# Kernel optimization log

Hardware: AMD Instinct MI355X
Metric: run time of the kernel (lower is better)

## Reference

```python
import jax, jax.numpy as jnp
import numpy as np

V, E, H, Z = 32000, 512, 1024, 256
B, S, T = 64, 256, 64
BOS_ID, EOS_ID = 1, 2


def gru_cell(x_gates, h, W_hh, b_hh):
    # torch GRU gate order: r, z, n. x_gates: (B,3H) precomputed W_ih@x+b_ih.
    hg = h @ W_hh.T + b_hh
    xr, xz, xn = jnp.split(x_gates, 3, axis=-1)
    hr, hz, hn = jnp.split(hg, 3, axis=-1)
    r = jax.nn.sigmoid(xr + hr)
    z = jax.nn.sigmoid(xz + hz)
    n = jnp.tanh(xn + r * hn)
    return (1.0 - z) * n + z * h


def setup_inputs() -> dict:
    key = jax.random.key(0)
    ks = jax.random.split(key, 24)
    u = lambda k, sh: jax.random.uniform(k, sh, jnp.float32, -0.1, 0.1)
    n = lambda k, sh: jax.random.normal(k, sh, jnp.float32) * 0.05
    inp = {
        'input': jax.random.randint(ks[0], (S, B), 0, V),
        'eps': jax.random.normal(ks[1], (B, Z), jnp.float32),
        'emb_enc': u(ks[2], (V, E)).at[0].set(0.0),  # padding_idx=0
        'Wih_e': n(ks[3], (3 * H, E)), 'Whh_e': n(ks[4], (3 * H, H)),
        'bih_e': n(ks[5], (3 * H,)), 'bhh_e': n(ks[6], (3 * H,)),
        'W_enc': n(ks[7], (Z, H)), 'b_enc': n(ks[8], (Z,)),
        'W_loc': n(ks[9], (Z, Z)), 'b_loc': n(ks[10], (Z,)),
        'W_scale': n(ks[11], (Z, Z)), 'b_scale': n(ks[12], (Z,)),
        'emb_dec': u(ks[13], (V, E)).at[0].set(0.0),
        'W_dec': n(ks[14], (H, Z)), 'b_dec': n(ks[15], (H,)),
        'Wih_d': n(ks[16], (3 * H, E)), 'Whh_d': n(ks[17], (3 * H, H)),
        'bih_d': n(ks[18], (3 * H,)), 'bhh_d': n(ks[19], (3 * H,)),
        'W_voc': n(ks[20], (V, H)), 'b_voc': n(ks[21], (V,)),
    }
    return inp


def reference(input, eps, emb_enc, Wih_e, Whh_e, bih_e, bhh_e,
              W_enc, b_enc, W_loc, b_loc, W_scale, b_scale,
              emb_dec, W_dec, b_dec, Wih_d, Whh_d, bih_d, bhh_d,
              W_voc, b_voc):
    # ---- encode ----
    x = emb_enc[input]                                   # (S,B,E)
    gx = jnp.einsum('sbe,ge->sbg', x, Wih_e) + bih_e     # (S,B,3H)
    h0 = jnp.zeros((B, H), x.dtype)
    h_last, _ = jax.lax.scan(lambda h, g: (gru_cell(g, h, Whh_e, bhh_e), None), h0, gx)
    henc = h_last @ W_enc.T + b_enc                      # (B,Z)
    loc = henc @ W_loc.T + b_loc
    scale = jax.nn.softplus(henc @ W_scale.T + b_scale)
    # ---- reparametrize ----
    z = loc + eps * jnp.exp(0.5 * scale)
    # ---- decode (fixed T steps; original loop is data-dependent on EOS) ----
    hidden = z @ W_dec.T + b_dec                         # (B,H)
    xd = jnp.broadcast_to(emb_dec[EOS_ID], (B, E))       # constant EOS input each step
    gxd = xd @ Wih_d.T + bih_d                           # (B,3H), hoisted out of loop

    def step(h, _):
        h2 = gru_cell(gxd, h, Whh_d, bhh_d)
        log_p = jax.nn.log_softmax(h2 @ W_voc.T + b_voc, axis=-1)  # (B,V)
        tok = jnp.argmax(log_p)  # global flat argmax, as torch.argmax(...).item()
        return h2, (log_p, tok)

    _, (log_p, toks) = jax.lax.scan(step, hidden, None, length=T)
    seq = jnp.concatenate([jnp.array([BOS_ID], toks.dtype), toks])
    return log_p, seq, loc, scale
```

## Files before the change

kernel.cpp:

```cpp
#include <hip/hip_runtime.h>
#include <math.h>
#include <stdint.h>
#include <stddef.h>

typedef unsigned short u16;
typedef unsigned int   u32;
typedef __attribute__((ext_vector_type(8))) short short8;
typedef __attribute__((ext_vector_type(4))) float f32x4;

#define DI __device__ __forceinline__

static constexpr int Vv = 32000, Ee = 512, Hh = 1024, Zz = 256;
static constexpr int Bb = 64, Ss = 256, Tt = 64;
static constexpr int G3 = 3 * Hh;

static constexpr size_t OFF_WHHE  = 0;
static constexpr size_t SZ_WHH    = (size_t)G3 * Hh * 2;
static constexpr size_t OFF_WHHD  = OFF_WHHE + SZ_WHH;
static constexpr size_t OFF_WIHE3 = OFF_WHHD + SZ_WHH;
static constexpr size_t SZ_WIHE3  = (size_t)G3 * (3 * Ee) * 2;
static constexpr size_t OFF_WVOC  = OFF_WIHE3 + SZ_WIHE3;
static constexpr size_t SZ_WVOC   = (size_t)Vv * Hh * 2;
static constexpr size_t OFF_XS    = OFF_WVOC + SZ_WVOC;
static constexpr size_t SZ_XS     = (size_t)Ss * Bb * (3 * Ee) * 2;
static constexpr size_t OFF_GX    = OFF_XS + SZ_XS;
static constexpr size_t SZ_GX     = (size_t)Ss * Bb * G3 * 4;
static constexpr size_t OFF_H2B   = OFF_GX;
static constexpr size_t OFF_H2F   = OFF_GX + SZ_GX;
static constexpr size_t SZ_H2F    = (size_t)Tt * Bb * Hh * 4;
static constexpr size_t OFF_H     = OFF_H2F + SZ_H2F;
static constexpr size_t OFF_GXD   = OFF_H + (size_t)Bb * Hh * 4;
static constexpr size_t OFF_HENC  = OFF_GXD + 12288;
static constexpr size_t OFF_ZB    = OFF_HENC + (size_t)Bb * Zz * 4;
static constexpr size_t OFF_RM    = OFF_ZB + (size_t)Bb * Zz * 4;
static constexpr size_t OFF_SE    = OFF_RM + 16384;
static constexpr size_t OFF_LSE   = OFF_SE + 16384;
static constexpr size_t OFF_BV    = OFF_LSE + 16384;
static constexpr size_t OFF_BI    = OFF_BV + 16384;
static constexpr size_t OFF_CC    = OFF_BI + 16384;
static constexpr size_t OFF_CAND  = OFF_CC + 16384;
static constexpr size_t OFF_BAR   = OFF_CAND + (size_t)4096 * 32 * 4;

static constexpr size_t SZ_HAB    = (size_t)Bb * 2 * Hh * 2;

DI u16 f2bf(float f) {
  u32 u = __float_as_uint(f);
  u32 r = (u + 0x7FFFu + ((u >> 16) & 1u)) >> 16;
  return (u16)r;
}
DI float bf2f(u16 h) { return __uint_as_float(((u32)h) << 16); }

DI f32x4 mfma16(short8 a, short8 b, f32x4 c) {
  return __builtin_amdgcn_mfma_f32_16x16x32_bf16(a, b, c, 0, 0, 0);
}
DI void llds16(const u16* g, u16* l) {
  __builtin_amdgcn_global_load_lds(
      (const __attribute__((address_space(1))) u32*)g,
      (__attribute__((address_space(3))) u32*)l, 16, 0, 0);
}

DI void ag_store_u32(u32* p, u32 v) {
  __hip_atomic_store(p, v, __ATOMIC_RELAXED, __HIP_MEMORY_SCOPE_AGENT);
}

DI u16* hbuf_dev(char* rA, char* rB, char* rC, int i) {
  if (i < 192) return (u16*)(rA + (size_t)i * SZ_HAB);
  if (i < 228) return (u16*)(rB + (size_t)(i - 192) * SZ_HAB);
  return (u16*)(rC + (size_t)(i - 228) * SZ_HAB);
}

__global__ void k_zero(u32* p, int n) {
  for (int i = blockIdx.x * 256 + threadIdx.x; i < n; i += gridDim.x * 256) p[i] = 0;
}

__global__ void k_trip(const float* __restrict__ W, u16* __restrict__ W3, int rows, int kin) {
  int n = rows * kin;
  for (int i = blockIdx.x * 256 + threadIdx.x; i < n; i += gridDim.x * 256) {
    int rr = i / kin, k = i - rr * kin;
    float v = W[i];
    u16 hi = f2bf(v);
    u16 lo = f2bf(v - bf2f(hi));
    u16* o = W3 + (size_t)rr * (3 * kin);
    o[k] = hi; o[kin + k] = hi; o[2 * kin + k] = lo;
  }
}

__global__ void k_tobf(const float* __restrict__ W, u16* __restrict__ Wb, int n) {
  for (int i = blockIdx.x * 256 + threadIdx.x; i < n; i += gridDim.x * 256) Wb[i] = f2bf(W[i]);
}

__global__ void k_xsplit(const int* __restrict__ inp, const float* __restrict__ emb,
                         u16* __restrict__ xs) {
  int n = Ss * Bb * Ee;
  for (int i = blockIdx.x * 256 + threadIdx.x; i < n; i += gridDim.x * 256) {
    int m = i >> 9, k = i & (Ee - 1);
    int tok = inp[m];
    float v = emb[(size_t)tok * Ee + k];
    u16 hi = f2bf(v);
    u16 lo = f2bf(v - bf2f(hi));
    u16* o = xs + (size_t)m * (3 * Ee);
    o[k] = hi; o[Ee + k] = lo; o[2 * Ee + k] = hi;
  }
}

__global__ void k_gxd(const float* __restrict__ emb_dec, const float* __restrict__ Wih_d,
                      const float* __restrict__ bih_d, float* __restrict__ gxd) {
  int g = blockIdx.x * 256 + threadIdx.x;
  if (g >= G3) return;
  const float* er = emb_dec + 2 * Ee;
  const float* wr = Wih_d + (size_t)g * Ee;
  float s = 0.f;
  for (int e = 0; e < Ee; e++) s += er[e] * wr[e];
  gxd[g] = s + bih_d[g];
}

__global__ __launch_bounds__(256, 2) void gemm_bt(
    const u16* __restrict__ A, const u16* __restrict__ Bw, const float* __restrict__ bias,
    float* __restrict__ C, int M, int N, int K) {
  __shared__ __align__(16) u16 As[128 * 32];
  __shared__ __align__(16) u16 Bs[128 * 32];
  int tid = threadIdx.x;
  int wave = tid >> 6, lane = tid & 63;
  int wr = wave >> 1, wc = wave & 1;
  int m0 = blockIdx.y * 128, n0 = blockIdx.x * 128;
  f32x4 acc[4][4];
#pragma unroll
  for (int i = 0; i < 4; i++)
#pragma unroll
    for (int j = 0; j < 4; j++) acc[i][j] = (f32x4){0.f, 0.f, 0.f, 0.f};

  int lrow = lane >> 2, lcol = (lane & 3) * 8;
  int r15 = lane & 15, kk = (lane >> 4) * 8;

  for (int k0 = 0; k0 < K; k0 += 32) {
    __syncthreads();
#pragma unroll
    for (int rch = 0; rch < 2; rch++) {
      int c = rch * 4 + wave;
      int row = c * 16 + lrow;
      llds16(A  + (size_t)(m0 + row) * K + k0 + lcol, &As[c * 512]);
      llds16(Bw + (size_t)(n0 + row) * K + k0 + lcol, &Bs[c * 512]);
    }
    __syncthreads();
    short8 af[4], bfv[4];
#pragma unroll
    for (int mi = 0; mi < 4; mi++)
      af[mi] = *(const short8*)&As[(wr * 64 + mi * 16 + r15) * 32 + kk];
#pragma unroll
    for (int ni = 0; ni < 4; ni++)
      bfv[ni] = *(const short8*)&Bs[(wc * 64 + ni * 16 + r15) * 32 + kk];
#pragma unroll
    for (int mi = 0; mi < 4; mi++)
#pragma unroll
      for (int ni = 0; ni < 4; ni++) acc[mi][ni] = mfma16(af[mi], bfv[ni], acc[mi][ni]);
  }
#pragma unroll
  for (int mi = 0; mi < 4; mi++)
#pragma unroll
    for (int ni = 0; ni < 4; ni++) {
      int col = n0 + wc * 64 + ni * 16 + r15;
      float bs = bias[col];
#pragma unroll
      for (int i = 0; i < 4; i++) {
        int row = m0 + wr * 64 + mi * 16 + (lane >> 4) * 4 + i;
        C[(size_t)row * N + col] = acc[mi][ni][i] + bs;
      }
    }
}

template <int DEC>
__global__ __launch_bounds__(512, 1) void k_pers(
    const u16* __restrict__ W, const float* __restrict__ bhh, const float* __restrict__ gx0,
    char* rA, char* rB, char* rC, float* Hst, float* h2f0, u16* h2b0, int* bar) {
  int tid = threadIdx.x, wave = tid >> 6, lane = tid & 63;
  int r15 = lane & 15, kk = (lane >> 4) * 8;
  int bq = blockIdx.x & 3, jt = blockIdx.x >> 2;
  int b0 = bq * 16, j0 = jt * 16;
  int kbase = wave * 128;
  const int NSTEP = DEC ? Tt : Ss;

  __shared__ float sC[8][64][13];
  __shared__ float hT[256];
  __shared__ __align__(8) u16 stg[2][16][16];

  int bl = tid >> 4, jc = tid & 15;
  float br = 0.f, bz = 0.f, bn = 0.f;
  float xr = 0.f, xz = 0.f, xn = 0.f;
  if (tid < 256) {
    hT[tid] = DEC ? Hst[(size_t)(b0 + bl) * Hh + j0 + jc] : 0.f;
    int j = j0 + jc;
    br = bhh[j]; bz = bhh[Hh + j]; bn = bhh[2 * Hh + j];
    if (DEC) { xr = gx0[j]; xz = gx0[Hh + j]; xn = gx0[2 * Hh + j]; }
    else {
      const float* gr = gx0 + (size_t)(b0 + bl) * G3;
      xr = gr[j]; xz = gr[Hh + j]; xn = gr[2 * Hh + j];
    }
  }
  __syncthreads();

  const u16* Wrow = W + (size_t)(j0 + r15) * Hh + kbase + kk;
  int lsrc = (bl >> 2) * 16 + jc;
  int isrc = bl & 3;

  for (int st = 0; st < NSTEP; st++) {
    const u16* hin = hbuf_dev(rA, rB, rC, st);

    f32x4 acc[3];
#pragma unroll
    for (int g = 0; g < 3; g++) acc[g] = (f32x4){0.f, 0.f, 0.f, 0.f};
    const u16* Ab = hin + (size_t)(b0 + r15) * 2048 + kbase + kk;
#pragma unroll
    for (int ks = 0; ks < 4; ks++) {
      int ko = ks * 32;
      short8 ah = *(const short8*)(Ab + ko);
      short8 al = *(const short8*)(Ab + 1024 + ko);
      short8 w0 = *(const short8*)(Wrow + ko);
      short8 w1 = *(const short8*)(Wrow + (size_t)Hh * Hh + ko);
      short8 w2 = *(const short8*)(Wrow + (size_t)2 * Hh * Hh + ko);
      acc[0] = mfma16(ah, w0, acc[0]);
      acc[1] = mfma16(ah, w1, acc[1]);
      acc[2] = mfma16(ah, w2, acc[2]);
      acc[0] = mfma16(al, w0, acc[0]);
      acc[1] = mfma16(al, w1, acc[1]);
      acc[2] = mfma16(al, w2, acc[2]);
    }
#pragma unroll
    for (int g = 0; g < 3; g++)
#pragma unroll
      for (int i = 0; i < 4; i++) sC[wave][lane][g * 4 + i] = acc[g][i];
    __syncthreads();

    if (tid < 256) {
      float hgr = br, hgz = bz, hgn = bn;
#pragma unroll
      for (int w = 0; w < 8; w++) {
        hgr += sC[w][lsrc][isrc];
        hgz += sC[w][lsrc][4 + isrc];
        hgn += sC[w][lsrc][8 + isrc];
      }
      float rg = 1.0f / (1.0f + expf(-(xr + hgr)));
      float zg = 1.0f / (1.0f + expf(-(xz + hgz)));
      float ng = tanhf(xn + rg * hgn);
      float hn = (1.0f - zg) * ng + zg * hT[tid];
      hT[tid] = hn;
      u16 hi = f2bf(hn), lo = f2bf(hn - bf2f(hi));
      stg[0][bl][jc] = hi;
      stg[1][bl][jc] = lo;
      if (DEC) h2f0[((size_t)st * Bb + b0 + bl) * Hh + j0 + jc] = hn;
    }
    __syncthreads();

    if (tid < 256) {
      int part = tid >> 7, idx = tid & 127, row = idx >> 3, dw = idx & 7;
      if (st + 1 < NSTEP) {
        u16* hout = hbuf_dev(rA, rB, rC, st + 1);
        u32 val = ((const u32*)&stg[part][row][0])[dw];
        ag_store_u32((u32*)(hout + (size_t)(b0 + row) * 2048 + part * 1024 + j0) + dw, val);
      }
      if (DEC && tid < 128) {
        u16* h2b = h2b0 + (size_t)st * Bb * Hh;
        ((u32*)(h2b + (size_t)(b0 + row) * Hh + j0))[dw] = ((const u32*)&stg[0][row][0])[dw];
      }
    }

    if (st + 1 < NSTEP) {
      asm volatile("s_waitcnt vmcnt(0)" ::: "memory");
      __syncthreads();
      if (!DEC && tid < 256) {
        const float* gr = gx0 + ((size_t)(st + 1) * Bb + b0 + bl) * G3;
        int j = j0 + jc;
        xr = gr[j]; xz = gr[Hh + j]; xn = gr[2 * Hh + j];
      }
      if (tid == 0) {
        int g = blockIdx.x & 7;
        int old = __hip_atomic_fetch_add(&bar[g * 16], 1,
                                         __ATOMIC_RELAXED, __HIP_MEMORY_SCOPE_AGENT);
        if (old == 32 * (st + 1) - 1)
          __hip_atomic_fetch_add(&bar[128 + bq * 16], 1,
                                 __ATOMIC_RELAXED, __HIP_MEMORY_SCOPE_AGENT);
        while (__hip_atomic_load(&bar[128 + bq * 16],
                                 __ATOMIC_RELAXED, __HIP_MEMORY_SCOPE_AGENT) < 2 * (st + 1))
          __builtin_amdgcn_s_sleep(1);
      }
      __syncthreads();
    }
  }

  if (!DEC && tid < 256)
    Hst[(size_t)(b0 + bl) * Hh + j0 + jc] = hT[tid];
}

template <int DEC>
__global__ __launch_bounds__(512, 1) void k_step3(
    const u16* __restrict__ W, const float* __restrict__ bhh, const float* __restrict__ gxp,
    const u16* __restrict__ hAin, u16* __restrict__ hAout, float* __restrict__ h,
    float* __restrict__ h2f, u16* __restrict__ h2b) {
  __shared__ float sC[4][64][13];
  int tid = threadIdx.x, wave = tid >> 6, lane = tid & 63;
  int mw = wave & 3, khalf = wave >> 2;
  int m0 = mw * 16;
  int r15 = lane & 15, kk = (lane >> 4) * 8;
  int j0 = blockIdx.x * 16;
  int kbase = khalf * 512;

  f32x4 acc[3];
#pragma unroll
  for (int g = 0; g < 3; g++) acc[g] = (f32x4){0.f, 0.f, 0.f, 0.f};

  const u16* Ah = hAin + (size_t)(m0 + r15) * 2048 + kbase + kk;
  const u16* Wr = W + (size_t)(j0 + r15) * Hh + kbase + kk;
#pragma unroll 4
  for (int ks = 0; ks < 16; ks++) {
    int ko = ks * 32;
    short8 ah = *(const short8*)(Ah + ko);
    short8 al = *(const short8*)(Ah + 1024 + ko);
    short8 b0 = *(const short8*)(Wr + ko);
    short8 b1 = *(const short8*)(Wr + (size_t)Hh * Hh + ko);
    short8 b2 = *(const short8*)(Wr + (size_t)2 * Hh * Hh + ko);
    acc[0] = mfma16(ah, b0, acc[0]);
    acc[1] = mfma16(ah, b1, acc[1]);
    acc[2] = mfma16(ah, b2, acc[2]);
    acc[0] = mfma16(al, b0, acc[0]);
    acc[1] = mfma16(al, b1, acc[1]);
    acc[2] = mfma16(al, b2, acc[2]);
  }

  if (khalf == 1) {
#pragma unroll
    for (int g = 0; g < 3; g++)
#pragma unroll
      for (int i = 0; i < 4; i++) sC[mw][lane][g * 4 + i] = acc[g][i];
  }
  __syncthreads();
  if (khalf == 1) return;

  int j = j0 + r15;
  float br = bhh[j], bz = bhh[Hh + j], bn = bhh[2 * Hh + j];
  float xrD = 0.f, xzD = 0.f, xnD = 0.f;
  if (DEC) { xrD = gxp[j]; xzD = gxp[Hh + j]; xnD = gxp[2 * Hh + j]; }
#pragma unroll
  for (int i = 0; i < 4; i++) {
    int b = m0 + (lane >> 4) * 4 + i;
    float hgr = acc[0][i] + sC[mw][lane][i]     + br;
    float hgz = acc[1][i] + sC[mw][lane][4 + i] + bz;
    float hgn = acc[2][i] + sC[mw][lane][8 + i] + bn;
    float xr, xz, xn;
    if (DEC) { xr = xrD; xz = xzD; xn = xnD; }
    else {
      const float* gr = gxp + (size_t)b * G3;
      xr = gr[j]; xz = gr[Hh + j]; xn = gr[2 * Hh + j];
    }
    float rg = 1.0f / (1.0f + expf(-(xr + hgr)));
    float zg = 1.0f / (1.0f + expf(-(xz + hgz)));
    float ng = tanhf(xn + rg * hgn);
    float hold = h[(size_t)b * Hh + j];
    float hn = (1.0f - zg) * ng + zg * hold;
    h[(size_t)b * Hh + j] = hn;
    u16 hi = f2bf(hn);
    u16 lo = f2bf(hn - bf2f(hi));
    hAout[(size_t)b * 2048 + j] = hi;
    hAout[(size_t)b * 2048 + 1024 + j] = lo;
    if (DEC) {
      h2f[(size_t)b * Hh + j] = hn;
      h2b[(size_t)b * Hh + j] = hi;
    }
  }
}

__global__ __launch_bounds__(256, 2) void k_head1(const float* __restrict__ h,
    const float* __restrict__ Wenc, const float* __restrict__ benc, float* __restrict__ henc) {
  int b = blockIdx.x;
  __shared__ float hs[Hh];
  for (int k = threadIdx.x; k < Hh; k += 256) hs[k] = h[(size_t)b * Hh + k];
  __syncthreads();
  int q = threadIdx.x;
  const float* wrw = Wenc + (size_t)q * Hh;
  float s = 0.f;
  for (int k = 0; k < Hh; k++) s += hs[k] * wrw[k];
  henc[b * Zz + q] = s + benc[q];
}

__global__ __launch_bounds__(256, 2) void k_head2(const float* __restrict__ henc,
    const float* __restrict__ Wloc, const float* __restrict__ bloc,
    const float* __restrict__ Wsc, const float* __restrict__ bsc,
    const float* __restrict__ eps, float* __restrict__ outLoc, float* __restrict__ outSc,
    float* __restrict__ zb) {
  int b = blockIdx.x;
  __shared__ float hs[Zz];
  if (threadIdx.x < Zz) hs[threadIdx.x] = henc[b * Zz + threadIdx.x];
  __syncthreads();
  int q = threadIdx.x;
  const float* wl = Wloc + (size_t)q * Zz;
  const float* wsp = Wsc + (size_t)q * Zz;
  float sl = 0.f, ssum = 0.f;
  for (int k = 0; k < Zz; k++) { sl += hs[k] * wl[k]; ssum += hs[k] * wsp[k]; }
  sl += bloc[q]; ssum += bsc[q];
  float sp = fmaxf(ssum, 0.f) + log1pf(expf(-fabsf(ssum)));
  float zv = sl + eps[b * Zz + q] * expf(0.5f * sp);
  outLoc[b * Zz + q] = sl;
  outSc[b * Zz + q] = sp;
  zb[b * Zz + q] = zv;
}

__global__ __launch_bounds__(256, 2) void k_head3(const float* __restrict__ zb,
    const float* __restrict__ Wdec, const float* __restrict__ bdec,
    float* __restrict__ h, u16* __restrict__ hA0) {
  int b = blockIdx.x;
  __shared__ float zs[Zz];
  if (threadIdx.x < Zz) zs[threadIdx.x] = zb[b * Zz + threadIdx.x];
  __syncthreads();
  for (int j = threadIdx.x; j < Hh; j += 256) {
    const float* wrw = Wdec + (size_t)j * Zz;
    float s = 0.f;
    for (int k = 0; k < Zz; k++) s += zs[k] * wrw[k];
    s += bdec[j];
    h[(size_t)b * Hh + j] = s;
    u16 hi = f2bf(s);
    u16 lo = f2bf(s - bf2f(hi));
    hA0[(size_t)b * 2048 + j] = hi;
    hA0[(size_t)b * 2048 + 1024 + j] = lo;
  }
}

__global__ __launch_bounds__(256, 2) void k_rowred(const float* __restrict__ logits,
    float* __restrict__ rowmax, float* __restrict__ sumexp, int* __restrict__ ccnt,
    int* __restrict__ cand) {
  int r = blockIdx.x;
  const float* row = logits + (size_t)r * Vv;
  __shared__ float red[4];
  __shared__ float srm;
  __shared__ int lcnt;
  __shared__ int lcand[32];
  int tid = threadIdx.x, wave = tid >> 6, lane = tid & 63;
  if (tid == 0) lcnt = 0;
  float m = -3.0e38f;
  for (int c = tid * 4; c < Vv; c += 1024) {
    f32x4 v = *(const f32x4*)(row + c);
    m = fmaxf(fmaxf(fmaxf(m, v.x), v.y), fmaxf(v.z, v.w));
  }
  for (int o = 32; o; o >>= 1) m = fmaxf(m, __shfl_xor(m, o));
  if (lane == 0) red[wave] = m;
  __syncthreads();
  if (tid == 0) srm = fmaxf(fmaxf(red[0], red[1]), fmaxf(red[2], red[3]));
  __syncthreads();
  float rm = srm;
  float s = 0.f;
  for (int c = tid * 4; c < Vv; c += 1024) {
    f32x4 v = *(const f32x4*)(row + c);
    s += expf(v.x - rm) + expf(v.y - rm) + expf(v.z - rm) + expf(v.w - rm);
    if (v.x >= rm - 0.0625f) { int sl = atomicAdd(&lcnt, 1); if (sl < 32) lcand[sl] = c; }
    if (v.y >= rm - 0.0625f) { int sl = atomicAdd(&lcnt, 1); if (sl < 32) lcand[sl] = c + 1; }
    if (v.z >= rm - 0.0625f) { int sl = atomicAdd(&lcnt, 1); if (sl < 32) lcand[sl] = c + 2; }
    if (v.w >= rm - 0.0625f) { int sl = atomicAdd(&lcnt, 1); if (sl < 32) lcand[sl] = c + 3; }
  }
  for (int o = 32; o; o >>= 1) s += __shfl_xor(s, o);
  if (lane == 0) red[wave] = s;
  __syncthreads();
  if (tid == 0) {
    float st = red[0] + red[1] + red[2] + red[3];
    int cc = lcnt < 32 ? lcnt : 32;
    for (int i = 0; i < cc; i++)
      for (int k2 = i + 1; k2 < cc; k2++)
        if (lcand[k2] < lcand[i]) { int t = lcand[i]; lcand[i] = lcand[k2]; lcand[k2] = t; }
    rowmax[r] = rm; sumexp[r] = st; ccnt[r] = cc;
    for (int i = 0; i < cc; i++) cand[r * 32 + i] = lcand[i];
  }
}

__global__ __launch_bounds__(256, 1) void k_refine(const float* __restrict__ logits,
    const float* __restrict__ h2f, const float* __restrict__ Wvoc, const float* __restrict__ bvoc,
    const float* __restrict__ rowmax, const float* __restrict__ sumexp,
    const int* __restrict__ ccnt, const int* __restrict__ cand,
    float* __restrict__ lsec, float* __restrict__ bestv, int* __restrict__ besti) {
  int r = blockIdx.x;
  __shared__ float hrow[Hh];
  __shared__ float lex[32];
  __shared__ float del[32];
  int tid = threadIdx.x, wave = tid >> 6, lane = tid & 63;
  for (int k = tid; k < Hh; k += 256) hrow[k] = h2f[(size_t)r * Hh + k];
  int cnt = ccnt[r];
  float rm = rowmax[r];
  __syncthreads();
  for (int ci = wave; ci < cnt; ci += 4) {
    int v = cand[r * 32 + ci];
    const float* wrw = Wvoc + (size_t)v * Hh;
    float s = 0.f;
    for (int k = lane; k < Hh; k += 64) s += hrow[k] * wrw[k];
    for (int o = 32; o; o >>= 1) s += __shfl_xor(s, o);
    if (lane == 0) {
      float le = s + bvoc[v];
      lex[ci] = le;
      float la = logits[(size_t)r * Vv + v];
      del[ci] = expf(le - rm) - expf(la - rm);
    }
  }
  __syncthreads();
  if (tid == 0) {
    float se = sumexp[r];
    for (int i = 0; i < cnt; i++) se += del[i];
    float lse = rm + logf(se);
    lsec[r] = lse;
    float bv = -3.0e38f; int bvi = 0;
    for (int i = 0; i < cnt; i++)
      if (lex[i] > bv) { bv = lex[i]; bvi = cand[r * 32 + i]; }
    bestv[r] = bv - lse;
    besti[r] = (r & 63) * Vv + bvi;
  }
}

__global__ void k_argmax(const float* __restrict__ bestv, const int* __restrict__ besti,
                         float* __restrict__ outseq) {
  int tid = threadIdx.x;
  if (tid == 0) outseq[0] = 1.0f;
  for (int t = 0; t < Tt; t++) {
    float v = bestv[t * 64 + tid];
    int ii = besti[t * 64 + tid];
    for (int o = 1; o < 64; o <<= 1) {
      float ov = __shfl_xor(v, o);
      int oi = __shfl_xor(ii, o);
      if (ov > v || (ov == v && oi < ii)) { v = ov; ii = oi; }
    }
    if (tid == 0) outseq[1 + t] = (float)ii;
  }
}

__global__ __launch_bounds__(256, 2) void k_logp(float* __restrict__ logits,
                                                 const float* __restrict__ lsec) {
  size_t total = (size_t)Tt * Bb * Vv / 4;
  for (size_t p = (size_t)blockIdx.x * 256 + threadIdx.x; p < total;
       p += (size_t)gridDim.x * 256) {
    int r = (int)(p / (Vv / 4));
    f32x4 v = *(f32x4*)(logits + p * 4);
    float l = lsec[r];
    v.x -= l; v.y -= l; v.z -= l; v.w -= l;
    *(f32x4*)(logits + p * 4) = v;
  }
}

extern "C" void kernel_launch(void* const* d_in, const int* in_sizes, int n_in,
                              void* d_out, int out_size, void* d_ws, size_t ws_size,
                              hipStream_t stream) {
  (void)in_sizes; (void)n_in; (void)out_size; (void)ws_size;
  const int*   inp     = (const int*)d_in[0];
  const float* eps     = (const float*)d_in[1];
  const float* emb_enc = (const float*)d_in[2];
  const float* Wih_e   = (const float*)d_in[3];
  const float* Whh_e   = (const float*)d_in[4];
  const float* bih_e   = (const float*)d_in[5];
  const float* bhh_e   = (const float*)d_in[6];
  const float* W_enc   = (const float*)d_in[7];
  const float* b_enc   = (const float*)d_in[8];
  const float* W_loc   = (const float*)d_in[9];
  const float* b_loc   = (const float*)d_in[10];
  const float* W_sc    = (const float*)d_in[11];
  const float* b_sc    = (const float*)d_in[12];
  const float* emb_dec = (const float*)d_in[13];
  const float* W_dec   = (const float*)d_in[14];
  const float* b_dec   = (const float*)d_in[15];
  const float* Wih_d   = (const float*)d_in[16];
  const float* Whh_d   = (const float*)d_in[17];
  const float* bih_d   = (const float*)d_in[18];
  const float* bhh_d   = (const float*)d_in[19];
  const float* W_voc   = (const float*)d_in[20];
  const float* b_voc   = (const float*)d_in[21];

  char* ws = (char*)d_ws;
  u16*   WHHE  = (u16*)(ws + OFF_WHHE);
  u16*   WHHD  = (u16*)(ws + OFF_WHHD);
  u16*   WIHE3 = (u16*)(ws + OFF_WIHE3);
  u16*   WVOC  = (u16*)(ws + OFF_WVOC);
  u16*   XS    = (u16*)(ws + OFF_XS);
  float* GX    = (float*)(ws + OFF_GX);
  float* Hst   = (float*)(ws + OFF_H);
  float* H2F   = (float*)(ws + OFF_H2F);
  u16*   H2B   = (u16*)(ws + OFF_H2B);
  float* GXD   = (float*)(ws + OFF_GXD);
  float* HENC  = (float*)(ws + OFF_HENC);
  float* ZB    = (float*)(ws + OFF_ZB);
  float* RM    = (float*)(ws + OFF_RM);
  float* SE    = (float*)(ws + OFF_SE);
  float* LSE   = (float*)(ws + OFF_LSE);
  float* BV    = (float*)(ws + OFF_BV);
  int*   BI    = (int*)(ws + OFF_BI);
  int*   CC    = (int*)(ws + OFF_CC);
  int*   CAND  = (int*)(ws + OFF_CAND);
  int*   BAR   = (int*)(ws + OFF_BAR);

  char* rA = ws + OFF_XS;
  char* rB = ws + OFF_WIHE3;
  char* rC = ws + OFF_H2F;
  auto hbuf = [&](int i) -> u16* {
    if (i < 192) return (u16*)(rA + (size_t)i * SZ_HAB);
    if (i < 228) return (u16*)(rB + (size_t)(i - 192) * SZ_HAB);
    return (u16*)(rC + (size_t)(i - 228) * SZ_HAB);
  };

  float* out     = (float*)d_out;
  float* logits  = out;
  float* outseq  = out + (size_t)Tt * Bb * Vv;
  float* outloc  = outseq + (Tt + 1);
  float* outsc   = outloc + Bb * Zz;

  k_tobf<<<1024, 256, 0, stream>>>(Whh_e, WHHE, G3 * Hh);
  k_tobf<<<1024, 256, 0, stream>>>(Whh_d, WHHD, G3 * Hh);
  k_trip<<<512, 256, 0, stream>>>(Wih_e, WIHE3, G3, Ee);
  k_tobf<<<2048, 256, 0, stream>>>(W_voc, WVOC, Vv * Hh);
  k_xsplit<<<2048, 256, 0, stream>>>(inp, emb_enc, XS);

  {
    dim3 g(G3 / 128, (Ss * Bb) / 128);
    gemm_bt<<<g, 256, 0, stream>>>(XS, WIHE3, bih_e, GX, Ss * Bb, G3, 3 * Ee);
  }
  k_gxd<<<12, 256, 0, stream>>>(emb_dec, Wih_d, bih_d, GXD);
  k_zero<<<64, 256, 0, stream>>>((u32*)hbuf(0), (int)(SZ_HAB / 4));
  k_zero<<<1, 256, 0, stream>>>((u32*)BAR, 256);

  hipError_t ce;
  {
    const u16* a0 = WHHE; const float* a1 = bhh_e; const float* a2 = GX;
    char* a3 = rA; char* a4 = rB; char* a5 = rC; float* a6 = Hst;
    float* a7 = nullptr; u16* a8 = nullptr; int* a9 = BAR;
    void* args[] = {&a0,&a1,&a2,&a3,&a4,&a5,&a6,&a7,&a8,&a9};
    ce = hipLaunchCooperativeKernel(reinterpret_cast<void*>(&k_pers<0>),
                                    dim3(256), dim3(512), args, 0, stream);
  }
  if (ce != hipSuccess) {
    for (int s = 0; s < Ss; s++)
      k_step3<0><<<64, 512, 0, stream>>>(WHHE, bhh_e, GX + (size_t)s * Bb * G3,
                                         hbuf(s), hbuf(s + 1), Hst, nullptr, nullptr);
  }

  k_head1<<<64, 256, 0, stream>>>(Hst, W_enc, b_enc, HENC);
  k_head2<<<64, 256, 0, stream>>>(HENC, W_loc, b_loc, W_sc, b_sc, eps, outloc, outsc, ZB);
  k_head3<<<64, 256, 0, stream>>>(ZB, W_dec, b_dec, Hst, hbuf(0));
  k_zero<<<1, 256, 0, stream>>>((u32*)BAR, 256);

  {
    const u16* a0 = WHHD; const float* a1 = bhh_d; const float* a2 = GXD;
    char* a3 = rA; char* a4 = rB; char* a5 = rC; float* a6 = Hst;
    float* a7 = H2F; u16* a8 = H2B; int* a9 = BAR;
    void* args[] = {&a0,&a1,&a2,&a3,&a4,&a5,&a6,&a7,&a8,&a9};
    hipError_t cd = hipLaunchCooperativeKernel(reinterpret_cast<void*>(&k_pers<1>),
                                               dim3(256), dim3(512), args, 0, stream);
    if (cd != hipSuccess) {
      for (int t = 0; t < Tt; t++)
        k_step3<1><<<64, 512, 0, stream>>>(WHHD, bhh_d, GXD, hbuf(t), hbuf(t + 1), Hst,
                                           H2F + (size_t)t * Bb * Hh,
                                           H2B + (size_t)t * Bb * Hh);
    }
  }

  {
    dim3 g(Vv / 128, (Tt * Bb) / 128);
    gemm_bt<<<g, 256, 0, stream>>>(H2B, WVOC, b_voc, logits, Tt * Bb, Vv, Hh);
  }

  k_rowred<<<Tt * Bb, 256, 0, stream>>>(logits, RM, SE, CC, CAND);
  k_refine<<<Tt * Bb, 256, 0, stream>>>(logits, H2F, W_voc, b_voc, RM, SE, CC, CAND, LSE, BV, BI);
  k_argmax<<<1, 64, 0, stream>>>(BV, BI, outseq);
  k_logp<<<2048, 256, 0, stream>>>(logits, LSE);
}
```

Baseline: 2.879 ms.

## Replace atomic-counter grid barrier with per-block flags and per-quarter gather

The persistent GRU kernel's inter-block barrier changes from two-level fetch_add counters to per-block step flags. Block jt==0 of each batch quarter has one wave poll all 64 peer flags and then publish a release flag, which the other blocks of that quarter spin on. The aim is to cut atomic read-modify-write contention and serialization on each of the 256 or 64 recurrent steps. Stores of h2f/h2b become agent-scope atomic stores, and the barrier buffer grows to 4224 words, which must fit inside the reserved workspace region.

```diff
diff --git a/kernel.cpp b/kernel.cpp
--- a/kernel.cpp
+++ b/kernel.cpp
@@ -62,6 +62,12 @@
 DI void ag_store_u32(u32* p, u32 v) {
   __hip_atomic_store(p, v, __ATOMIC_RELAXED, __HIP_MEMORY_SCOPE_AGENT);
 }
+DI u32 ag_load_u32(const u32* p) {
+  return __hip_atomic_load((u32*)p, __ATOMIC_RELAXED, __HIP_MEMORY_SCOPE_AGENT);
+}
+DI void ag_store_f32(float* p, float v) {
+  __hip_atomic_store(p, v, __ATOMIC_RELAXED, __HIP_MEMORY_SCOPE_AGENT);
+}
 
 DI u16* hbuf_dev(char* rA, char* rB, char* rC, int i) {
   if (i < 192) return (u16*)(rA + (size_t)i * SZ_HAB);
@@ -171,7 +177,7 @@
 template <int DEC>
 __global__ __launch_bounds__(512, 1) void k_pers(
     const u16* __restrict__ W, const float* __restrict__ bhh, const float* __restrict__ gx0,
-    char* rA, char* rB, char* rC, float* Hst, float* h2f0, u16* h2b0, int* bar) {
+    char* rA, char* rB, char* rC, float* Hst, float* h2f0, u16* h2b0, u32* bar) {
   int tid = threadIdx.x, wave = tid >> 6, lane = tid & 63;
   int r15 = lane & 15, kk = (lane >> 4) * 8;
   int bq = blockIdx.x & 3, jt = blockIdx.x >> 2;
@@ -201,6 +207,7 @@
   const u16* Wrow = W + (size_t)(j0 + r15) * Hh + kbase + kk;
   int lsrc = (bl >> 2) * 16 + jc;
   int isrc = bl & 3;
+  int flgidx = (lane * 4 + bq) * 16;
 
   for (int st = 0; st < NSTEP; st++) {
     const u16* hin = hbuf_dev(rA, rB, rC, st);
@@ -246,7 +253,7 @@
       u16 hi = f2bf(hn), lo = f2bf(hn - bf2f(hi));
       stg[0][bl][jc] = hi;
       stg[1][bl][jc] = lo;
-      if (DEC) h2f0[((size_t)st * Bb + b0 + bl) * Hh + j0 + jc] = hn;
+      if (DEC) ag_store_f32(&h2f0[((size_t)st * Bb + b0 + bl) * Hh + j0 + jc], hn);
     }
     __syncthreads();
 
@@ -259,27 +266,32 @@
       }
       if (DEC && tid < 128) {
         u16* h2b = h2b0 + (size_t)st * Bb * Hh;
-        ((u32*)(h2b + (size_t)(b0 + row) * Hh + j0))[dw] = ((const u32*)&stg[0][row][0])[dw];
+        ag_store_u32((u32*)(h2b + (size_t)(b0 + row) * Hh + j0) + dw,
+                     ((const u32*)&stg[0][row][0])[dw]);
       }
     }
 
     if (st + 1 < NSTEP) {
       asm volatile("s_waitcnt vmcnt(0)" ::: "memory");
       __syncthreads();
+      if (tid == 0)
+        ag_store_u32(&bar[blockIdx.x * 16], (u32)(st + 1));
       if (!DEC && tid < 256) {
         const float* gr = gx0 + ((size_t)(st + 1) * Bb + b0 + bl) * G3;
         int j = j0 + jc;
         xr = gr[j]; xz = gr[Hh + j]; xn = gr[2 * Hh + j];
       }
-      if (tid == 0) {
-        int g = blockIdx.x & 7;
-        int old = __hip_atomic_fetch_add(&bar[g * 16], 1,
-                                         __ATOMIC_RELAXED, __HIP_MEMORY_SCOPE_AGENT);
-        if (old == 32 * (st + 1) - 1)
-          __hip_atomic_fetch_add(&bar[128 + bq * 16], 1,
-                                 __ATOMIC_RELAXED, __HIP_MEMORY_SCOPE_AGENT);
-        while (__hip_atomic_load(&bar[128 + bq * 16],
-                                 __ATOMIC_RELAXED, __HIP_MEMORY_SCOPE_AGENT) < 2 * (st + 1))
+      if (jt == 0) {
+        if (wave == 0) {
+          for (;;) {
+            int v = (int)ag_load_u32(&bar[flgidx]);
+            if (__all(v >= st + 1)) break;
+            __builtin_amdgcn_s_sleep(1);
+          }
+          if (lane == 0) ag_store_u32(&bar[4096 + bq * 16], (u32)(st + 1));
+        }
+      } else if (tid == 0) {
+        while ((int)ag_load_u32(&bar[4096 + bq * 16]) < st + 1)
           __builtin_amdgcn_s_sleep(1);
       }
       __syncthreads();
@@ -584,7 +596,7 @@
   int*   BI    = (int*)(ws + OFF_BI);
   int*   CC    = (int*)(ws + OFF_CC);
   int*   CAND  = (int*)(ws + OFF_CAND);
-  int*   BAR   = (int*)(ws + OFF_BAR);
+  u32*   BAR   = (u32*)(ws + OFF_BAR);
 
   char* rA = ws + OFF_XS;
   char* rB = ws + OFF_WIHE3;
@@ -613,13 +625,13 @@
   }
   k_gxd<<<12, 256, 0, stream>>>(emb_dec, Wih_d, bih_d, GXD);
   k_zero<<<64, 256, 0, stream>>>((u32*)hbuf(0), (int)(SZ_HAB / 4));
-  k_zero<<<1, 256, 0, stream>>>((u32*)BAR, 256);
+  k_zero<<<1, 256, 0, stream>>>(BAR, 4224);
 
   hipError_t ce;
   {
     const u16* a0 = WHHE; const float* a1 = bhh_e; const float* a2 = GX;
     char* a3 = rA; char* a4 = rB; char* a5 = rC; float* a6 = Hst;
-    float* a7 = nullptr; u16* a8 = nullptr; int* a9 = BAR;
+    float* a7 = nullptr; u16* a8 = nullptr; u32* a9 = BAR;
     void* args[] = {&a0,&a1,&a2,&a3,&a4,&a5,&a6,&a7,&a8,&a9};
     ce = hipLaunchCooperativeKernel(reinterpret_cast<void*>(&k_pers<0>),
                                     dim3(256), dim3(512), args, 0, stream);
@@ -633,12 +645,12 @@
   k_head1<<<64, 256, 0, stream>>>(Hst, W_enc, b_enc, HENC);
   k_head2<<<64, 256, 0, stream>>>(HENC, W_loc, b_loc, W_sc, b_sc, eps, outloc, outsc, ZB);
   k_head3<<<64, 256, 0, stream>>>(ZB, W_dec, b_dec, Hst, hbuf(0));
-  k_zero<<<1, 256, 0, stream>>>((u32*)BAR, 256);
+  k_zero<<<1, 256, 0, stream>>>(BAR, 4224);
 
   {
     const u16* a0 = WHHD; const float* a1 = bhh_d; const float* a2 = GXD;
     char* a3 = rA; char* a4 = rB; char* a5 = rC; float* a6 = Hst;
-    float* a7 = H2F; u16* a8 = H2B; int* a9 = BAR;
+    float* a7 = H2F; u16* a8 = H2B; u32* a9 = BAR;
     void* args[] = {&a0,&a1,&a2,&a3,&a4,&a5,&a6,&a7,&a8,&a9};
     hipError_t cd = hipLaunchCooperativeKernel(reinterpret_cast<void*>(&k_pers<1>),
                                                dim3(256), dim3(512), args, 0, stream);
```

Result: no change. 2.825 ms (-1.9%).
